# Performance work log

Hardware: AMD Instinct MI355X
Metric: run time of the kernel (lower is better)

Reference implementation:

```python
import jax
jax.config.update("jax_enable_x64", True)
import jax.numpy as jnp
import numpy as np

# NTT-friendly stand-in prime for BLS12-377 Fr (residues fit in int64, products in 62 bits)
P = 2013265921          # 15 * 2^27 + 1
GEN = 31                # generator of (Z/P)^*
COSET = 7               # coset shift generator
LOG_DOMAIN = 21
DOMAIN = 1 << LOG_DOMAIN
BATCH = 8


def _pow_table(base, length):
    """numpy int64 table [base^0, ..., base^(length-1)] mod P, built by doubling."""
    t = np.ones(length, dtype=np.int64)
    k = 1
    while k < length:
        mult = pow(int(base), k, P)          # exact python-int exponentiation
        end = min(2 * k, length)
        t[k:end] = (t[:end - k] * mult) % P  # < 2^62, no overflow
        k = end
    return t


def _bitrev(n):
    b = int(n).bit_length() - 1
    idx = np.arange(n, dtype=np.int64)
    rev = np.zeros(n, dtype=np.int64)
    for i in range(b):
        rev |= ((idx >> i) & 1) << (b - 1 - i)
    return rev


def _ntt_core(x, inverse):
    """Iterative radix-2 Cooley-Tukey NTT over rows of x: [batch, n] int64 residues mod P."""
    b, n = x.shape
    logn = n.bit_length() - 1
    root = pow(GEN, (P - 1) // n, P)         # primitive n-th root of unity
    if inverse:
        root = pow(root, P - 2, P)
    wpow = _pow_table(root, n // 2)          # root^j, j < n/2 (host-side, exact)
    x = x[:, jnp.asarray(_bitrev(n))]        # bit-reversal permutation
    for s in range(1, logn + 1):             # structural loop over log2(n) stages
        m = 1 << s
        half = m >> 1
        tw = jnp.asarray(wpow[:: n // m][:half])   # stage twiddles root^{j*n/m}
        xr = x.reshape(b, n // m, m)
        e, o = xr[..., :half], xr[..., half:]
        t = (o * tw) % P                     # butterfly: vectorized over all groups
        x = jnp.concatenate([(e + t) % P, (e - t) % P], axis=-1).reshape(b, n)
    return x


def setup_inputs() -> dict:
    key = jax.random.key(0)
    inp = jax.random.randint(key, (BATCH, DOMAIN), 0, P, dtype=jnp.int64)
    return {"input": inp, "is_intt": 0, "is_coset": 0}


def reference(input, is_intt, is_coset):
    x = jnp.mod(input, P)
    n = x.shape[-1]
    if (not is_intt) and is_coset:
        # coset NTT: multiply element i by COSET^i before the forward transform
        x = (x * jnp.asarray(_pow_table(COSET, n))) % P
    x = _ntt_core(x, inverse=bool(is_intt))
    if is_intt:
        if is_coset:
            # coset INTT: undo the coset shift after the inverse transform
            x = (x * jnp.asarray(_pow_table(pow(COSET, P - 2, P), n))) % P
        n_inv = pow(int(n), P - 2, P)
        x = (x * n_inv) % P                  # scale by n^{-1}
    return x
```

## Files before the change

### kernel.cpp

```cpp
#include <hip/hip_runtime.h>
#include <stdint.h>

typedef unsigned int u32;
typedef unsigned long long u64;

#define MOD_P 2013265921u

#define T_A      0
#define T_B      16384
#define T_W128P  32768
#define T_RP     49152
#define T_CLP    49216
#define T_CHP    65600
#define T_NINV   65728

__device__ __forceinline__ u32 mul64mod(u32 a, u32 b){ return (u32)((u64)a * b % MOD_P); }

__device__ u32 powmod(u32 b, u32 e){
  u32 r = 1;
  while (e){ if (e & 1) r = mul64mod(r, b); b = mul64mod(b, b); e >>= 1; }
  return r;
}

__device__ __forceinline__ u32 shoup_of(u32 v){ return (u32)(((u64)v << 32) / MOD_P); }

__device__ __forceinline__ u32 redP(u32 a){
  u32 b = a - MOD_P;
  return b < a ? b : a;
}

__device__ __forceinline__ u32 mul_shoup(u32 a, uint2 t){
  u32 q = __umulhi(a, t.y);
  u32 r = a * t.x - q * MOD_P;
  return redP(r);
}

__device__ __forceinline__ constexpr int rev4(int m){
  return ((m&1)<<3) | ((m&2)<<1) | ((m&4)>>1) | ((m&8)>>3);
}

__device__ __forceinline__ void bf(u32 &x, u32 &y, uint2 t){
  u32 s = redP(x + y);
  u32 d = x - y + MOD_P;
  x = s; y = mul_shoup(d, t);
}
__device__ __forceinline__ void bf0(u32 &x, u32 &y){
  u32 s = redP(x + y);
  u32 d = x - y + MOD_P;
  x = s; y = d;
}

__device__ __forceinline__ void stages_p1(u32 v[16], int b, const uint2* __restrict__ twl){
  #pragma unroll
  for (int m = 0; m < 8; ++m) bf(v[m], v[m+8], twl[b + 8*m]);
  #pragma unroll
  for (int g = 0; g < 2; ++g)
    #pragma unroll
    for (int m = 0; m < 4; ++m) bf(v[g*8+m], v[g*8+m+4], twl[(b + 8*m) << 1]);
  #pragma unroll
  for (int g = 0; g < 4; ++g)
    #pragma unroll
    for (int m = 0; m < 2; ++m) bf(v[g*4+m], v[g*4+m+2], twl[(b + 8*m) << 2]);
  #pragma unroll
  for (int k = 0; k < 8; ++k) bf(v[2*k], v[2*k+1], twl[b << 3]);
}
__device__ __forceinline__ void stages_p2(u32 v[16], const uint2* __restrict__ twl){
  #pragma unroll
  for (int g = 0; g < 2; ++g)
    #pragma unroll
    for (int m = 0; m < 4; ++m) bf(v[g*8+m], v[g*8+m+4], twl[m << 4]);
  #pragma unroll
  for (int g = 0; g < 4; ++g)
    #pragma unroll
    for (int m = 0; m < 2; ++m) bf(v[g*4+m], v[g*4+m+2], twl[m << 5]);
  #pragma unroll
  for (int k = 0; k < 8; ++k) bf0(v[2*k], v[2*k+1]);
}

extern "C" __global__ void k_gen(uint2* __restrict__ tw, const int* __restrict__ f_intt){
  const int idx = blockIdx.x * 256 + threadIdx.x;
  const int intt = f_intt[0];
  u32 w = powmod(31u, (MOD_P - 1) >> 21);
  if (intt) w = powmod(w, MOD_P - 2);
  const u32 w128 = powmod(w, 128u);
  const int hi = idx >> 7, lo = idx & 127;

  u32 a = powmod(w, (u32)(hi * lo));
  tw[T_A + idx] = make_uint2(a, shoup_of(a));
  u32 b = powmod(w128, (u32)(hi * lo));
  tw[T_B + idx] = make_uint2(b, shoup_of(b));
  u32 v2 = powmod(w128, (u32)idx);
  tw[T_W128P + idx] = make_uint2(v2, shoup_of(v2));
  u32 c = intt ? powmod(7u, MOD_P - 2) : 7u;
  u32 cv = powmod(c, (u32)idx);
  tw[T_CLP + idx] = make_uint2(cv, shoup_of(cv));
  if (idx < 128){
    u32 h = powmod(c, (u32)idx << 14);
    tw[T_CHP + idx] = make_uint2(h, shoup_of(h));
  }
  if (idx < 64){
    u32 rv = powmod(powmod(w, 1u << 14), (u32)idx);
    tw[T_RP + idx] = make_uint2(rv, shoup_of(rv));
  }
  if (idx == 0){
    u32 ninv = powmod(1u << 21, MOD_P - 2);
    tw[T_NINV] = make_uint2(ninv, shoup_of(ninv));
  }
}

extern "C" __global__ void __launch_bounds__(1024, 8) k_passA(
    const u32* __restrict__ x, u32* __restrict__ y, const uint2* __restrict__ tw,
    const int* __restrict__ f_intt, const int* __restrict__ f_coset)
{
  __shared__ u32 lds[16384];
  const int wg = blockIdx.x;
  const int jb = wg & 127;
  const int batch = wg >> 7;
  const int t = threadIdx.x;
  const int jc = t & 127;
  const int b = __builtin_amdgcn_readfirstlane(t >> 7);
  const u32* xb = x + ((size_t)batch << 21);
  u32* yb = y + ((size_t)batch << 21);
  const uint2* twl = tw + T_RP;

  u32 v[16];
  #pragma unroll
  for (int m = 0; m < 16; ++m){
    u32 a = xb[((size_t)(b + 8*m) << 14) + (jb << 7) + jc];
    v[m] = redP(a);
  }
  if ((f_intt[0] == 0) && (f_coset[0] != 0)){
    uint2 cl = tw[T_CLP + (jb << 7) + jc];
    #pragma unroll
    for (int m = 0; m < 16; ++m){
      v[m] = mul_shoup(v[m], cl);
      v[m] = mul_shoup(v[m], tw[T_CHP + b + 8*m]);
    }
  }
  stages_p1(v, b, twl);
  #pragma unroll
  for (int m = 0; m < 16; ++m) lds[((b + 8*m) << 7) | jc] = v[m];
  __syncthreads();
  #pragma unroll
  for (int m = 0; m < 16; ++m) v[m] = lds[((16*b + m) << 7) | jc];
  stages_p2(v, twl);
  const int rb = ((b&1)<<2) | (b&2) | ((b&4)>>2);
  #pragma unroll
  for (int m = 0; m < 16; ++m){
    const int ka = (rev4(m) << 3) | rb;
    u32 vv = mul_shoup(v[m], tw[T_A + (ka << 7) + jc]);
    vv = mul_shoup(vv, tw[T_W128P + ka * jb]);
    yb[((size_t)ka << 14) + (jb << 7) + jc] = vv;
  }
}

extern "C" __global__ void __launch_bounds__(1024, 8) k_passB(
    u32* __restrict__ y, const uint2* __restrict__ tw)
{
  __shared__ u32 lds[16384];
  const int wg = blockIdx.x;
  const int ka = wg & 127;
  const int batch = wg >> 7;
  const int t = threadIdx.x;
  const int jc = t & 127;
  const int b = __builtin_amdgcn_readfirstlane(t >> 7);
  u32* yb = y + ((size_t)batch << 21) + ((size_t)ka << 14);
  const uint2* twl = tw + T_RP;

  u32 v[16];
  #pragma unroll
  for (int m = 0; m < 16; ++m) v[m] = yb[((b + 8*m) << 7) + jc];
  stages_p1(v, b, twl);
  #pragma unroll
  for (int m = 0; m < 16; ++m) lds[((b + 8*m) << 7) | jc] = v[m];
  __syncthreads();
  #pragma unroll
  for (int m = 0; m < 16; ++m) v[m] = lds[((16*b + m) << 7) | jc];
  stages_p2(v, twl);
  const int rb = ((b&1)<<2) | (b&2) | ((b&4)>>2);
  #pragma unroll
  for (int m = 0; m < 16; ++m){
    const int kb = (rev4(m) << 3) | rb;
    u32 vv = mul_shoup(v[m], tw[T_B + (kb << 7) + jc]);
    yb[(kb << 7) + jc] = vv;
  }
}

__device__ __forceinline__ int cidx(int row, int a){
  return (row << 7) | (a ^ (row >> 2));
}
extern "C" __global__ void __launch_bounds__(1024, 8) k_passC(
    u32* __restrict__ y, const uint2* __restrict__ tw,
    const int* __restrict__ f_intt, const int* __restrict__ f_coset)
{
  __shared__ u32 lds[16384];
  const int wg = blockIdx.x;
  const int kb = wg & 127;
  const int batch = wg >> 7;
  u32* yb = y + ((size_t)batch << 21);
  const u32* base = yb + (kb << 7);
  const int t = threadIdx.x;
  {
    const int q = t & 31;
    const int rr = t >> 5;
    #pragma unroll
    for (int i = 0; i < 4; ++i){
      int kaL = rr + 32*i;
      uint4 v4 = *(const uint4*)(base + ((size_t)kaL << 14) + (q << 2));
      lds[cidx(4*q+0, kaL)] = v4.x;
      lds[cidx(4*q+1, kaL)] = v4.y;
      lds[cidx(4*q+2, kaL)] = v4.z;
      lds[cidx(4*q+3, kaL)] = v4.w;
    }
  }
  __syncthreads();
  const int a = t & 127;
  const int b = __builtin_amdgcn_readfirstlane(t >> 7);
  const uint2* twl = tw + T_RP;
  u32 v[16];
  #pragma unroll
  for (int m = 0; m < 16; ++m) v[m] = lds[cidx(b + 8*m, a)];
  stages_p1(v, b, twl);
  #pragma unroll
  for (int m = 0; m < 16; ++m) lds[cidx(b + 8*m, a)] = v[m];
  __syncthreads();
  #pragma unroll
  for (int m = 0; m < 16; ++m) v[m] = lds[cidx(16*b + m, a)];
  stages_p2(v, twl);
  const int rb = ((b&1)<<2) | (b&2) | ((b&4)>>2);
  const int intt = f_intt[0];
  const int coset = f_coset[0];
  #pragma unroll
  for (int m = 0; m < 16; ++m){
    const int kc = (rev4(m) << 3) | rb;
    u32 vv = v[m];
    if (intt){
      vv = mul_shoup(vv, tw[T_NINV]);
      if (coset){
        vv = mul_shoup(vv, tw[T_CLP + (kb << 7) + a]);
        vv = mul_shoup(vv, tw[T_CHP + kc]);
      }
    } else {
      vv = redP(vv);
    }
    yb[((size_t)kc << 14) + (kb << 7) + a] = vv;
  }
}

extern "C" void kernel_launch(void* const* d_in, const int* in_sizes, int n_in,
                              void* d_out, int out_size, void* d_ws, size_t ws_size,
                              hipStream_t stream)
{
  const u32* x = (const u32*)d_in[0];
  const int* f_intt  = (const int*)d_in[1];
  const int* f_coset = (const int*)d_in[2];
  u32* y   = (u32*)d_out;
  uint2* tw = (uint2*)d_ws;
  const int batch = in_sizes[0] >> 21;
  const int nwg = batch << 7;

  k_gen  <<<64,   256, 0, stream>>>(tw, f_intt);
  k_passA<<<nwg, 1024, 0, stream>>>(x, y, tw, f_intt, f_coset);
  k_passB<<<nwg, 1024, 0, stream>>>(y, tw);
  k_passC<<<nwg, 1024, 0, stream>>>(y, tw, f_intt, f_coset);
}
```

Before: 107.0 us.

## Parallelize twiddle generation per entry and stage global loads through LDS

The twiddle generator now has each thread compute exactly one table entry with a single powmod from the base generator. Inverses are folded in as exponent negation, replacing several long powmod chains per thread, and the launch grows to 257 blocks. Pass A and pass B now load input with coalesced 128-bit vector loads into LDS before the register butterflies, instead of strided scalar loads. Pass C writes its output with nontemporal stores. These target the latency-bound table setup and the memory efficiency of the passes, at the cost of an extra LDS round trip and barrier in A and B.

```diff
diff --git a/kernel.cpp b/kernel.cpp
--- a/kernel.cpp
+++ b/kernel.cpp
@@ -77,35 +77,45 @@
   for (int k = 0; k < 8; ++k) bf0(v[2*k], v[2*k+1]);
 }
 
+__device__ __forceinline__ int cidx(int row, int a){
+  return (row << 7) | (a ^ (row >> 2));
+}
+
 extern "C" __global__ void k_gen(uint2* __restrict__ tw, const int* __restrict__ f_intt){
-  const int idx = blockIdx.x * 256 + threadIdx.x;
+  const u32 tid = blockIdx.x * 256 + threadIdx.x;
   const int intt = f_intt[0];
-  u32 w = powmod(31u, (MOD_P - 1) >> 21);
-  if (intt) w = powmod(w, MOD_P - 2);
-  const u32 w128 = powmod(w, 128u);
-  const int hi = idx >> 7, lo = idx & 127;
-
-  u32 a = powmod(w, (u32)(hi * lo));
-  tw[T_A + idx] = make_uint2(a, shoup_of(a));
-  u32 b = powmod(w128, (u32)(hi * lo));
-  tw[T_B + idx] = make_uint2(b, shoup_of(b));
-  u32 v2 = powmod(w128, (u32)idx);
-  tw[T_W128P + idx] = make_uint2(v2, shoup_of(v2));
-  u32 c = intt ? powmod(7u, MOD_P - 2) : 7u;
-  u32 cv = powmod(c, (u32)idx);
-  tw[T_CLP + idx] = make_uint2(cv, shoup_of(cv));
-  if (idx < 128){
-    u32 h = powmod(c, (u32)idx << 14);
-    tw[T_CHP + idx] = make_uint2(h, shoup_of(h));
-  }
-  if (idx < 64){
-    u32 rv = powmod(powmod(w, 1u << 14), (u32)idx);
-    tw[T_RP + idx] = make_uint2(rv, shoup_of(rv));
-  }
-  if (idx == 0){
-    u32 ninv = powmod(1u << 21, MOD_P - 2);
-    tw[T_NINV] = make_uint2(ninv, shoup_of(ninv));
-  }
+  const u32 MASK = (1u << 21) - 1;
+  u32 v; int dst;
+  if (tid < 16384){
+    u32 e = (tid >> 7) * (tid & 127);
+    if (intt) e = ((1u<<21) - e) & MASK;
+    v = powmod(31u, 960u * e); dst = T_A + tid;
+  } else if (tid < 32768){
+    u32 i = tid - 16384;
+    u32 e = (((i >> 7) * (i & 127)) << 7) & MASK;
+    if (intt) e = ((1u<<21) - e) & MASK;
+    v = powmod(31u, 960u * e); dst = T_B + i;
+  } else if (tid < 49152){
+    u32 i = tid - 32768;
+    u32 e = (i << 7) & MASK;
+    if (intt) e = ((1u<<21) - e) & MASK;
+    v = powmod(31u, 960u * e); dst = T_W128P + i;
+  } else if (tid < 65536){
+    u32 i = tid - 49152;
+    v = intt ? powmod(7u, (MOD_P - 1 - i) % (MOD_P - 1)) : powmod(7u, i);
+    dst = T_CLP + i;
+  } else if (tid < 65664){
+    u32 e = (tid - 65536) << 14;
+    v = intt ? powmod(7u, MOD_P - 1 - e) : powmod(7u, e);
+    dst = T_CHP + (tid - 65536);
+  } else if (tid < 65728){
+    u32 e = ((tid - 65664) << 14) & MASK;
+    if (intt) e = ((1u<<21) - e) & MASK;
+    v = powmod(31u, 960u * e); dst = T_RP + (tid - 65664);
+  } else if (tid == 65728){
+    v = powmod(1u << 21, MOD_P - 2); dst = T_NINV;
+  } else return;
+  tw[dst] = make_uint2(v, shoup_of(v));
 }
 
 extern "C" __global__ void __launch_bounds__(1024, 8) k_passA(
@@ -117,18 +127,25 @@
   const int jb = wg & 127;
   const int batch = wg >> 7;
   const int t = threadIdx.x;
+  const u32* xb = x + ((size_t)batch << 21) + (jb << 7);
+  u32* yb = y + ((size_t)batch << 21);
+  const uint2* twl = tw + T_RP;
+  {
+    const int q = t & 31, rr = t >> 5;
+    #pragma unroll
+    for (int i = 0; i < 4; ++i){
+      const int ja = rr + 32*i;
+      uint4 v4 = *(const uint4*)(xb + ((size_t)ja << 14) + (q << 2));
+      u32* d = &lds[(ja << 7) | (q << 2)];
+      d[0] = redP(v4.x); d[1] = redP(v4.y); d[2] = redP(v4.z); d[3] = redP(v4.w);
+    }
+  }
+  __syncthreads();
   const int jc = t & 127;
   const int b = __builtin_amdgcn_readfirstlane(t >> 7);
-  const u32* xb = x + ((size_t)batch << 21);
-  u32* yb = y + ((size_t)batch << 21);
-  const uint2* twl = tw + T_RP;
-
   u32 v[16];
   #pragma unroll
-  for (int m = 0; m < 16; ++m){
-    u32 a = xb[((size_t)(b + 8*m) << 14) + (jb << 7) + jc];
-    v[m] = redP(a);
-  }
+  for (int m = 0; m < 16; ++m) v[m] = lds[((b + 8*m) << 7) | jc];
   if ((f_intt[0] == 0) && (f_coset[0] != 0)){
     uint2 cl = tw[T_CLP + (jb << 7) + jc];
     #pragma unroll
@@ -162,14 +179,20 @@
   const int ka = wg & 127;
   const int batch = wg >> 7;
   const int t = threadIdx.x;
+  u32* yb = y + ((size_t)batch << 21) + ((size_t)ka << 14);
+  const uint2* twl = tw + T_RP;
+  {
+    const uint4* s4 = (const uint4*)yb;
+    uint4* l4 = (uint4*)lds;
+    #pragma unroll
+    for (int i = 0; i < 4; ++i) l4[t + 1024*i] = s4[t + 1024*i];
+  }
+  __syncthreads();
   const int jc = t & 127;
   const int b = __builtin_amdgcn_readfirstlane(t >> 7);
-  u32* yb = y + ((size_t)batch << 21) + ((size_t)ka << 14);
-  const uint2* twl = tw + T_RP;
-
   u32 v[16];
   #pragma unroll
-  for (int m = 0; m < 16; ++m) v[m] = yb[((b + 8*m) << 7) + jc];
+  for (int m = 0; m < 16; ++m) v[m] = lds[((b + 8*m) << 7) | jc];
   stages_p1(v, b, twl);
   #pragma unroll
   for (int m = 0; m < 16; ++m) lds[((b + 8*m) << 7) | jc] = v[m];
@@ -186,9 +209,6 @@
   }
 }
 
-__device__ __forceinline__ int cidx(int row, int a){
-  return (row << 7) | (a ^ (row >> 2));
-}
 extern "C" __global__ void __launch_bounds__(1024, 8) k_passC(
     u32* __restrict__ y, const uint2* __restrict__ tw,
     const int* __restrict__ f_intt, const int* __restrict__ f_coset)
@@ -243,7 +263,7 @@
     } else {
       vv = redP(vv);
     }
-    yb[((size_t)kc << 14) + (kb << 7) + a] = vv;
+    __builtin_nontemporal_store(vv, yb + ((size_t)kc << 14) + (kb << 7) + a);
   }
 }
 
@@ -259,7 +279,7 @@
   const int batch = in_sizes[0] >> 21;
   const int nwg = batch << 7;
 
-  k_gen  <<<64,   256, 0, stream>>>(tw, f_intt);
+  k_gen  <<<257,  256, 0, stream>>>(tw, f_intt);
   k_passA<<<nwg, 1024, 0, stream>>>(x, y, tw, f_intt, f_coset);
   k_passB<<<nwg, 1024, 0, stream>>>(y, tw);
   k_passC<<<nwg, 1024, 0, stream>>>(y, tw, f_intt, f_coset);
```

Result: faster. 103.3 us (-3.4%).
